# Performance work log

Hardware: AMD Instinct MI355X
Metric: run time of the kernel (lower is better)

## Reference

```python
import jax, jax.numpy as jnp
import numpy as np

D_MODEL = 1024
N_HEADS = 16
HEAD_SIZE = D_MODEL // N_HEADS
D_FF = 4096
EPS = 1e-6


def _layernorm(x, g, b):
    # Faithful to source: (x + mean) / (std + eps), unbiased std (torch default)
    mean = jnp.mean(x, axis=-1, keepdims=True)
    std = jnp.std(x, axis=-1, keepdims=True, ddof=1)
    return g * ((x + mean) / (std + EPS)) + b


def setup_inputs() -> dict:
    key = jax.random.key(0)
    ks = jax.random.split(key, 12)
    s = lambda fan_in: 1.0 / np.sqrt(fan_in)
    x = jax.random.normal(ks[0], (4, 2048, D_MODEL), dtype=jnp.float32)
    Wq = jax.random.uniform(ks[1], (N_HEADS, D_MODEL, HEAD_SIZE), jnp.float32, -s(D_MODEL), s(D_MODEL))
    Wk = jax.random.uniform(ks[2], (N_HEADS, D_MODEL, HEAD_SIZE), jnp.float32, -s(D_MODEL), s(D_MODEL))
    Wv = jax.random.uniform(ks[3], (N_HEADS, D_MODEL, HEAD_SIZE), jnp.float32, -s(D_MODEL), s(D_MODEL))
    Wo = jax.random.uniform(ks[4], (D_MODEL, D_MODEL), jnp.float32, -s(D_MODEL), s(D_MODEL))
    bo = jax.random.uniform(ks[5], (D_MODEL,), jnp.float32, -s(D_MODEL), s(D_MODEL))
    W1 = jax.random.uniform(ks[6], (D_MODEL, D_FF), jnp.float32, -s(D_MODEL), s(D_MODEL))
    b1 = jax.random.uniform(ks[7], (D_FF,), jnp.float32, -s(D_MODEL), s(D_MODEL))
    W2 = jax.random.uniform(ks[8], (D_FF, D_MODEL), jnp.float32, -s(D_FF), s(D_FF))
    b2 = jax.random.uniform(ks[9], (D_MODEL,), jnp.float32, -s(D_FF), s(D_FF))
    g1 = jnp.ones((D_MODEL,), jnp.float32)
    be1 = jnp.zeros((D_MODEL,), jnp.float32)
    g2 = jnp.ones((D_MODEL,), jnp.float32)
    be2 = jnp.zeros((D_MODEL,), jnp.float32)
    return {"x": x, "Wq": Wq, "Wk": Wk, "Wv": Wv, "Wo": Wo, "bo": bo,
            "W1": W1, "b1": b1, "W2": W2, "b2": b2,
            "g1": g1, "be1": be1, "g2": g2, "be2": be2}


def reference(x, Wq, Wk, Wv, Wo, bo, W1, b1, W2, b2, g1, be1, g2, be2):
    # Multi-head attention; note: source scales by sqrt(d_model), not sqrt(head_size)
    scale = 1.0 / np.sqrt(D_MODEL)
    q = jnp.einsum('bsd,hde->bhse', x, Wq)
    k = jnp.einsum('bsd,hde->bhse', x, Wk)
    v = jnp.einsum('bsd,hde->bhse', x, Wv)
    scores = jnp.einsum('bhse,bhte->bhst', q, k) * scale
    attn = jax.nn.softmax(scores, axis=-1)
    o = jnp.einsum('bhst,bhte->bhse', attn, v)
    B, H, S, E = o.shape
    o = o.transpose(0, 2, 1, 3).reshape(B, S, H * E)  # concat heads
    mha_out = o @ Wo + bo

    h1 = _layernorm(x + mha_out, g1, be1)

    ff = jax.nn.relu(h1 @ W1 + b1) @ W2 + b2
    out = _layernorm(h1 + ff, g2, be2)
    return out
```

## Files before the change

### kernel.cpp

```cpp
#include <hip/hip_runtime.h>

typedef short short8 __attribute__((ext_vector_type(8)));
typedef short short4v __attribute__((ext_vector_type(4)));
typedef float floatx4 __attribute__((ext_vector_type(4)));

#define D_MODEL 1024
#define N_HEADS 16
#define HEAD    64
#define D_FF    4096
#define SEQ     2048
#define BATCH   4
#define TOKENS  (BATCH*SEQ)

__device__ __forceinline__ float b2f(unsigned short u) {
  return __uint_as_float(((unsigned)u) << 16);
}
__device__ __forceinline__ unsigned short f2b(float f) {
  unsigned u = __float_as_uint(f);
  unsigned r = 0x7fffu + ((u >> 16) & 1u);
  return (unsigned short)((u + r) >> 16);
}
__device__ __forceinline__ floatx4 mfma16(short8 a, short8 b, floatx4 c) {
  return __builtin_amdgcn_mfma_f32_16x16x32_bf16(a, b, c, 0, 0, 0);
}
__device__ __forceinline__ void load16_lds(const unsigned short* g, unsigned short* l) {
  __builtin_amdgcn_global_load_lds((const __attribute__((address_space(1))) void*)g,
                                   (__attribute__((address_space(3))) void*)l, 16, 0, 0);
}

__device__ __forceinline__ void transp_body(
    const float* __restrict__ src, unsigned short* __restrict__ dst,
    int R, int C, int bx, int by, float (*t)[65])
{
  int cb = bx * 64, rb = by * 64;
#pragma unroll
  for (int i = 0; i < 16; i++) {
    int idx = i * 256 + threadIdx.x;
    int lr = idx >> 6, lc = idx & 63;
    t[lr][lc] = src[(size_t)(rb + lr) * C + cb + lc];
  }
  __syncthreads();
#pragma unroll
  for (int i = 0; i < 16; i++) {
    int idx = i * 256 + threadIdx.x;
    int lc = idx >> 6, lr = idx & 63;
    dst[(size_t)(cb + lc) * R + rb + lr] = f2b(t[lr][lc]);
  }
}

__global__ __launch_bounds__(256) void prep_kernel(
    const float* __restrict__ x, unsigned short* __restrict__ x_bf,
    const float* __restrict__ Wq, const float* __restrict__ Wk,
    const float* __restrict__ Wv, unsigned short* __restrict__ qkv_bt,
    const float* __restrict__ Wo, unsigned short* __restrict__ wo_bt,
    const float* __restrict__ W1, unsigned short* __restrict__ w1_bt,
    const float* __restrict__ W2, unsigned short* __restrict__ w2_bt)
{
  __shared__ float t[64][65];
  int bid = blockIdx.x;
  if (bid < 8192) {
    int idx = bid * 1024 + threadIdx.x * 4;
    float4 v = *(const float4*)(x + idx);
    short4v o;
    o[0] = (short)f2b(v.x); o[1] = (short)f2b(v.y);
    o[2] = (short)f2b(v.z); o[3] = (short)f2b(v.w);
    *(short4v*)(x_bf + idx) = o;
  } else if (bid < 8960) {
    int by = bid - 8192;
    int xt = by & 15, z = by >> 4;
    int sel = z >> 4, h = z & 15;
    const float* W = (sel == 0) ? Wq : ((sel == 1) ? Wk : Wv);
    const float* src = W + (size_t)h * D_MODEL * HEAD;
    int rb = xt * 64;
#pragma unroll
    for (int i = 0; i < 16; i++) {
      int idx = i * 256 + threadIdx.x;
      int lr = idx >> 6, lc = idx & 63;
      t[lr][lc] = src[(size_t)(rb + lr) * HEAD + lc];
    }
    __syncthreads();
    unsigned short* d0 = qkv_bt + (size_t)(sel * 1024 + h * 64) * D_MODEL;
#pragma unroll
    for (int i = 0; i < 16; i++) {
      int idx = i * 256 + threadIdx.x;
      int lc = idx >> 6, lr = idx & 63;
      d0[(size_t)lc * D_MODEL + rb + lr] = f2b(t[lr][lc]);
    }
  } else if (bid < 9216) {
    int i = bid - 8960;
    transp_body(Wo, wo_bt, 1024, 1024, i & 15, i >> 4, t);
  } else if (bid < 10240) {
    int i = bid - 9216;
    transp_body(W1, w1_bt, 1024, 4096, i & 63, i >> 6, t);
  } else {
    int i = bid - 10240;
    transp_body(W2, w2_bt, 4096, 1024, i & 15, i >> 4, t);
  }
}

__global__ __launch_bounds__(256, 2) void gemm128(
    const unsigned short* __restrict__ A, const unsigned short* __restrict__ BT,
    const float* __restrict__ biasf, const float* __restrict__ residf,
    const unsigned short* __restrict__ residb, void* __restrict__ outp,
    int M, int N, int K, int epi)
{
  __shared__ unsigned short a_sh[2 * 128 * 32];
  __shared__ unsigned short b_sh[2 * 128 * 32];

  const int tid  = threadIdx.x;
  const int lane = tid & 63;
  const int wave = tid >> 6;
  const int quad = lane >> 4;
  const int l15  = lane & 15;
  const int wm   = wave & 1;
  const int wn   = wave >> 1;

  const int lin = blockIdx.y * gridDim.x + blockIdx.x;
  const int xcd = lin & 7, j = lin >> 3;
  const int m0 = (xcd * 8 + (j & 7)) * 128;
  const int n0 = (j >> 3) * 128;

  const int rA = tid >> 2;
  const int kc = (tid & 3) * 8;
  const unsigned short* ag0 = A  + (size_t)(m0 + rA) * K + kc;
  const unsigned short* ag1 = A  + (size_t)(m0 + rA + 64) * K + kc;
  const unsigned short* bg0 = BT + (size_t)(n0 + rA) * K + kc;
  const unsigned short* bg1 = BT + (size_t)(n0 + rA + 64) * K + kc;
  unsigned short* la0 = a_sh + wave * 512;
  unsigned short* la1 = a_sh + 2048 + wave * 512;
  unsigned short* lb0 = b_sh + wave * 512;
  unsigned short* lb1 = b_sh + 2048 + wave * 512;

  floatx4 acc[4][4] = {};

  for (int k0 = 0; k0 < K; k0 += 64) {
    __syncthreads();
    load16_lds(ag0 + k0, la0);
    load16_lds(ag1 + k0, la1);
    load16_lds(bg0 + k0, lb0);
    load16_lds(bg1 + k0, lb1);
    load16_lds(ag0 + k0 + 32, la0 + 4096);
    load16_lds(ag1 + k0 + 32, la1 + 4096);
    load16_lds(bg0 + k0 + 32, lb0 + 4096);
    load16_lds(bg1 + k0 + 32, lb1 + 4096);
    __syncthreads();
#pragma unroll
    for (int h = 0; h < 2; h++) {
      short8 aF[4], bF[4];
#pragma unroll
      for (int i = 0; i < 4; i++)
        aF[i] = *(const short8*)(a_sh + h * 4096 + (wm * 64 + i * 16 + l15) * 32 + quad * 8);
#pragma unroll
      for (int i = 0; i < 4; i++)
        bF[i] = *(const short8*)(b_sh + h * 4096 + (wn * 64 + i * 16 + l15) * 32 + quad * 8);
#pragma unroll
      for (int mi = 0; mi < 4; mi++)
#pragma unroll
        for (int ni = 0; ni < 4; ni++)
          acc[mi][ni] = mfma16(aF[mi], bF[ni], acc[mi][ni]);
    }
  }

#pragma unroll
  for (int mi = 0; mi < 4; mi++) {
#pragma unroll
    for (int ni = 0; ni < 4; ni++) {
      const int col = n0 + wn * 64 + ni * 16 + l15;
      const int row0 = m0 + wm * 64 + mi * 16 + quad * 4;
      if (epi == 0) {
        int sel = col >> 10;
        int cc = col & 1023;
        int h = cc >> 6, e = cc & 63;
        int b = row0 >> 11, s0 = row0 & 2047;
        if (sel < 2) {
          unsigned short* base = (unsigned short*)outp + (size_t)sel * 8388608;
#pragma unroll
          for (int r = 0; r < 4; r++) {
            float v2 = (sel == 0) ? acc[mi][ni][r] * 0.04508422f : acc[mi][ni][r];
            base[((size_t)((b * N_HEADS + h) * SEQ + (s0 + r))) * HEAD + e] = f2b(v2);
          }
        } else {
          unsigned short* base = (unsigned short*)outp + (size_t)2 * 8388608;
          short4v pk;
#pragma unroll
          for (int r = 0; r < 4; r++) pk[r] = (short)f2b(acc[mi][ni][r]);
          *(short4v*)(base + ((size_t)((b * N_HEADS + h) * HEAD + e)) * SEQ + s0) = pk;
        }
      } else if (epi == 1) {
#pragma unroll
        for (int r = 0; r < 4; r++)
          ((float*)outp)[(size_t)(row0 + r) * N + col] =
              acc[mi][ni][r] + biasf[col] + residf[(size_t)(row0 + r) * N + col];
      } else if (epi == 2) {
#pragma unroll
        for (int r = 0; r < 4; r++)
          ((unsigned short*)outp)[(size_t)(row0 + r) * N + col] =
              f2b(fmaxf(acc[mi][ni][r] + biasf[col], 0.0f));
      } else {
#pragma unroll
        for (int r = 0; r < 4; r++)
          ((float*)outp)[(size_t)(row0 + r) * N + col] =
              acc[mi][ni][r] + biasf[col] + b2f(residb[(size_t)(row0 + r) * N + col]);
      }
    }
  }
}

__global__ __launch_bounds__(512, 2) void gemm256(
    const unsigned short* __restrict__ A, const unsigned short* __restrict__ BT,
    const float* __restrict__ biasf, void* __restrict__ outp,
    int M, int N, int K, int epi)
{
  __shared__ unsigned short a_sh[2 * 256 * 64];
  __shared__ unsigned short b_sh[2 * 256 * 64];

  const int tid  = threadIdx.x;
  const int lane = tid & 63;
  const int wave = tid >> 6;
  const int quad = lane >> 4;
  const int l15  = lane & 15;
  const int wm   = wave >> 2;
  const int wn   = wave & 3;

  const int lin = blockIdx.y * gridDim.x + blockIdx.x;
  const int xcd = lin & 7, j = lin >> 3;
  const int m0 = (xcd * 4 + (j & 3)) * 256;
  const int n0 = (j >> 2) * 256;

  const int u  = tid >> 3;
  const int sc = (tid & 7) ^ (u & 7);
  const unsigned short* a_src = A  + (size_t)(m0 + u) * K + sc * 8;
  const int borig = ((u >> 5) * 64) + (u & 31);
  const unsigned short* b_src = BT + (size_t)(n0 + borig) * K + sc * 8;
  unsigned short* a_dst = a_sh + wave * 512;
  unsigned short* b_dst = b_sh + wave * 512;

#define SA(T, Rc)  load16_lds(a_src + (size_t)(Rc) * K + (T) * 64, \
                              a_dst + ((T) & 1) * 16384 + (Rc) * 64)
#define SB(T, Rb, Radd) load16_lds(b_src + (size_t)(Radd) * K + (T) * 64, \
                              b_dst + ((T) & 1) * 16384 + (Rb) * 64)
#define STG_A0(T) do { SA(T, 0);   SA(T, 128); } while (0)
#define STG_A1(T) do { SA(T, 64);  SA(T, 192); } while (0)
#define STG_B0(T) do { SB(T, 0, 0);    SB(T, 64, 128); } while (0)
#define STG_B1(T) do { SB(T, 128, 32); SB(T, 192, 160); } while (0)

  floatx4 acc[8][4] = {};
  short8 aF[4][2];
  short8 bF[2][2][2];
  const unsigned short* ash = a_sh;
  const unsigned short* bsh = b_sh;

#define LDA(QM) \
  _Pragma("unroll") for (int mi = 0; mi < 4; mi++) \
  _Pragma("unroll") for (int kh = 0; kh < 2; kh++) \
    aF[mi][kh] = *(const short8*)(ash + (wm * 128 + (QM) * 64 + mi * 16 + l15) * 64 \
                                  + (((kh * 4 + quad) ^ (l15 & 7)) * 8));
#define LDB(QN) \
  _Pragma("unroll") for (int ni = 0; ni < 2; ni++) \
  _Pragma("unroll") for (int kh = 0; kh < 2; kh++) \
    bF[QN][ni][kh] = *(const short8*)(bsh + ((QN) * 128 + wn * 32 + ni * 16 + l15) * 64 \
                                      + (((kh * 4 + quad) ^ (l15 & 7)) * 8));
#define MM(QM, QN) \
  _Pragma("unroll") for (int mi = 0; mi < 4; mi++) \
  _Pragma("unroll") for (int ni = 0; ni < 2; ni++) { \
    acc[(QM) * 4 + mi][(QN) * 2 + ni] = \
        mfma16(aF[mi][0], bF[QN][ni][0], acc[(QM) * 4 + mi][(QN) * 2 + ni]); \
    acc[(QM) * 4 + mi][(QN) * 2 + ni] = \
        mfma16(aF[mi][1], bF[QN][ni][1], acc[(QM) * 4 + mi][(QN) * 2 + ni]); \
  }
#define PH_VM(N) asm volatile("s_waitcnt vmcnt(" #N ")" ::: "memory");
#define PH_MID() \
  __builtin_amdgcn_s_barrier(); \
  asm volatile("s_waitcnt lgkmcnt(0)" ::: "memory"); \
  __builtin_amdgcn_sched_barrier(0); \
  __builtin_amdgcn_s_setprio(1);
#define PH_END() \
  __builtin_amdgcn_s_setprio(0); \
  __builtin_amdgcn_s_barrier();

  const int NT = K >> 6;

  STG_A0(0); STG_B0(0); STG_A1(0); STG_B1(0); STG_A0(1); STG_B0(1);
  PH_VM(4)
  __builtin_amdgcn_s_barrier();

  for (int t = 0; t < NT - 2; ++t) {
    ash = a_sh + (t & 1) * 16384;
    bsh = b_sh + (t & 1) * 16384;

    LDA(0) LDB(0)
    STG_A1(t + 1);
    PH_MID() MM(0, 0) PH_END();

    LDB(1)
    STG_B1(t + 1);
    PH_MID() MM(0, 1) PH_END();

    LDA(1)
    STG_A0(t + 2);
    PH_MID() MM(1, 0) PH_END();

    STG_B0(t + 2);
    PH_VM(4)
    PH_MID() MM(1, 1) PH_END();
  }
  {
    const int t = NT - 2;
    ash = a_sh + (t & 1) * 16384;
    bsh = b_sh + (t & 1) * 16384;

    LDA(0) LDB(0)
    STG_A1(t + 1);
    PH_MID() MM(0, 0) PH_END();

    LDB(1)
    STG_B1(t + 1);
    PH_MID() MM(0, 1) PH_END();

    LDA(1)
    PH_MID() MM(1, 0) PH_END();

    PH_VM(0)
    PH_MID() MM(1, 1) PH_END();
  }
  {
    const int t = NT - 1;
    ash = a_sh + (t & 1) * 16384;
    bsh = b_sh + (t & 1) * 16384;

    LDA(0) LDB(0)
    PH_MID() MM(0, 0) PH_END();

    LDB(1)
    PH_MID() MM(0, 1) PH_END();

    LDA(1)
    PH_MID() MM(1, 0) PH_END();

    PH_MID() MM(1, 1) PH_END();
  }

#undef SA
#undef SB
#undef STG_A0
#undef STG_A1
#undef STG_B0
#undef STG_B1
#undef LDA
#undef LDB
#undef MM
#undef PH_VM
#undef PH_MID
#undef PH_END

#pragma unroll
  for (int mi = 0; mi < 8; mi++) {
#pragma unroll
    for (int ni = 0; ni < 4; ni++) {
      const int col = n0 + wn * 64 + ni * 16 + l15;
      const int row0 = m0 + wm * 128 + mi * 16 + quad * 4;
      if (epi == 0) {
        int sel = col >> 10;
        int cc = col & 1023;
        int h = cc >> 6, e = cc & 63;
        int b = row0 >> 11, s0 = row0 & 2047;
        if (sel < 2) {
          unsigned short* base = (unsigned short*)outp + (size_t)sel * 8388608;
#pragma unroll
          for (int r = 0; r < 4; r++) {
            float v2 = (sel == 0) ? acc[mi][ni][r] * 0.04508422f : acc[mi][ni][r];
            base[((size_t)((b * N_HEADS + h) * SEQ + (s0 + r))) * HEAD + e] = f2b(v2);
          }
        } else {
          unsigned short* base = (unsigned short*)outp + (size_t)2 * 8388608;
          short4v pk;
#pragma unroll
          for (int r = 0; r < 4; r++) pk[r] = (short)f2b(acc[mi][ni][r]);
          *(short4v*)(base + ((size_t)((b * N_HEADS + h) * HEAD + e)) * SEQ + s0) = pk;
        }
      } else {
#pragma unroll
        for (int r = 0; r < 4; r++)
          ((unsigned short*)outp)[(size_t)(row0 + r) * N + col] =
              f2b(fmaxf(acc[mi][ni][r] + biasf[col], 0.0f));
      }
    }
  }
}

__global__ __launch_bounds__(256, 4) void attn_kernel(
    const unsigned short* __restrict__ q, const unsigned short* __restrict__ k,
    const unsigned short* __restrict__ vt, unsigned short* __restrict__ o)
{
  const int bh = blockIdx.y;
  const int qt = blockIdx.x;
  const int tid = threadIdx.x, lane = tid & 63, wave = tid >> 6;
  const int quad = lane >> 4, l15 = lane & 15;
  const size_t base = (size_t)bh * SEQ * HEAD;

  __shared__ unsigned short k_sh[64 * 64];
  __shared__ unsigned short vT_sh[64 * 64];
  __shared__ unsigned short p_sh[4 * 32 * 72];
  unsigned short* pw = p_sh + wave * 32 * 72;

  short8 qf[2][2];
#pragma unroll
  for (int mj = 0; mj < 2; mj++) {
    const unsigned short* qp =
        q + base + (size_t)(qt * 128 + wave * 32 + mj * 16 + l15) * HEAD;
    qf[mj][0] = *(const short8*)(qp + quad * 8);
    qf[mj][1] = *(const short8*)(qp + 32 + quad * 8);
  }

  floatx4 oacc[2][4] = {};
  floatx4 rsacc[2] = {};

  short8 onesf;
  {
    short ov = (l15 == 0) ? (short)0x3F80 : (short)0;
#pragma unroll
    for (int jj = 0; jj < 8; jj++) onesf[jj] = ov;
  }

  const int r8 = lane >> 3, slot = lane & 7;

  for (int kt = 0; kt < SEQ / 64; kt++) {
    __syncthreads();
#pragma unroll
    for (int i = 0; i < 2; i++) {
      int t = wave * 16 + i * 8 + r8;
      int cg = slot ^ (t & 7);
      load16_lds(k + base + (size_t)(kt * 64 + t) * HEAD + cg * 8,
                 k_sh + (wave * 16 + i * 8) * 64);
      load16_lds(vt + base + (size_t)t * SEQ + kt * 64 + cg * 8,
                 vT_sh + (wave * 16 + i * 8) * 64);
    }
    __syncthreads();

#pragma unroll
    for (int ti = 0; ti < 4; ti++) {
      int t = ti * 16 + l15;
      short8 kf0 = *(const short8*)(k_sh + t * 64 + ((quad ^ (t & 7)) * 8));
      short8 kf1 = *(const short8*)(k_sh + t * 64 + (((4 + quad) ^ (t & 7)) * 8));
      floatx4 s0 = {0.f, 0.f, 0.f, 0.f}, s1 = {0.f, 0.f, 0.f, 0.f};
      __builtin_amdgcn_s_setprio(1);
      s0 = mfma16(kf0, qf[0][0], s0);
      s0 = mfma16(kf1, qf[0][1], s0);
      s1 = mfma16(kf0, qf[1][0], s1);
      s1 = mfma16(kf1, qf[1][1], s1);
      __builtin_amdgcn_s_setprio(0);
#pragma unroll
      for (int mj = 0; mj < 2; mj++) {
        floatx4 s = mj ? s1 : s0;
        float p0 = __builtin_amdgcn_exp2f(s[0]);
        float p1 = __builtin_amdgcn_exp2f(s[1]);
        float p2 = __builtin_amdgcn_exp2f(s[2]);
        float p3 = __builtin_amdgcn_exp2f(s[3]);
        uint2 u;
        u.x = __builtin_amdgcn_perm(__float_as_uint(p1), __float_as_uint(p0), 0x07060302u);
        u.y = __builtin_amdgcn_perm(__float_as_uint(p3), __float_as_uint(p2), 0x07060302u);
        *(uint2*)(pw + (mj * 16 + l15) * 72 + ti * 16 + quad * 4) = u;
      }
    }

    {
      short8 pf[2][2];
#pragma unroll
      for (int mj = 0; mj < 2; mj++) {
        pf[mj][0] = *(const short8*)(pw + (mj * 16 + l15) * 72 + quad * 8);
        pf[mj][1] = *(const short8*)(pw + (mj * 16 + l15) * 72 + 32 + quad * 8);
      }
      __builtin_amdgcn_s_setprio(1);
#pragma unroll
      for (int ni = 0; ni < 4; ni++) {
        int e = ni * 16 + l15;
        short8 bv0 = *(const short8*)(vT_sh + e * 64 + ((quad ^ (e & 7)) * 8));
        short8 bv1 = *(const short8*)(vT_sh + e * 64 + (((4 + quad) ^ (e & 7)) * 8));
#pragma unroll
        for (int mj = 0; mj < 2; mj++) {
          oacc[mj][ni] = mfma16(pf[mj][0], bv0, oacc[mj][ni]);
          oacc[mj][ni] = mfma16(pf[mj][1], bv1, oacc[mj][ni]);
        }
      }
#pragma unroll
      for (int mj = 0; mj < 2; mj++) {
        rsacc[mj] = mfma16(pf[mj][0], onesf, rsacc[mj]);
        rsacc[mj] = mfma16(pf[mj][1], onesf, rsacc[mj]);
      }
      __builtin_amdgcn_s_setprio(0);
    }
  }

  const int b = bh >> 4, h = bh & 15;
#pragma unroll
  for (int mj = 0; mj < 2; mj++)
#pragma unroll
    for (int r = 0; r < 4; r++) {
      int s = qt * 128 + wave * 32 + mj * 16 + quad * 4 + r;
      float rsv = __shfl(rsacc[mj][r], quad * 16, 64);
      float inv = 1.0f / rsv;
#pragma unroll
      for (int ni = 0; ni < 4; ni++)
        o[((size_t)(b * SEQ + s)) * D_MODEL + h * HEAD + ni * 16 + l15] =
            f2b(oacc[mj][ni][r] * inv);
    }
}

__global__ __launch_bounds__(256) void ln_kernel(
    const float* __restrict__ in, const float* __restrict__ g,
    const float* __restrict__ be, void* __restrict__ outp, int write_bf16)
{
  const int row = blockIdx.x * 4 + (threadIdx.x >> 6);
  const int lane = threadIdx.x & 63;
  const float* xp = in + (size_t)row * D_MODEL;
  float4 xv[4];
  float s = 0.0f, ss = 0.0f;
#pragma unroll
  for (int j = 0; j < 4; j++) {
    xv[j] = *(const float4*)(xp + j * 256 + lane * 4);
    s += (xv[j].x + xv[j].y) + (xv[j].z + xv[j].w);
    ss += (xv[j].x * xv[j].x + xv[j].y * xv[j].y) +
          (xv[j].z * xv[j].z + xv[j].w * xv[j].w);
  }
#pragma unroll
  for (int m = 1; m < 64; m <<= 1) {
    s += __shfl_xor(s, m, 64);
    ss += __shfl_xor(ss, m, 64);
  }
  float mean = s * (1.0f / 1024.0f);
  float var = fmaxf((ss - 1024.0f * mean * mean) * (1.0f / 1023.0f), 0.0f);
  float inv = 1.0f / (sqrtf(var) + 1e-6f);
#pragma unroll
  for (int j = 0; j < 4; j++) {
    int c = j * 256 + lane * 4;
    float4 g4 = *(const float4*)(g + c);
    float4 b4 = *(const float4*)(be + c);
    float y0 = g4.x * ((xv[j].x + mean) * inv) + b4.x;
    float y1 = g4.y * ((xv[j].y + mean) * inv) + b4.y;
    float y2 = g4.z * ((xv[j].z + mean) * inv) + b4.z;
    float y3 = g4.w * ((xv[j].w + mean) * inv) + b4.w;
    if (write_bf16) {
      short4v o4;
      o4[0] = (short)f2b(y0); o4[1] = (short)f2b(y1);
      o4[2] = (short)f2b(y2); o4[3] = (short)f2b(y3);
      *(short4v*)((unsigned short*)outp + (size_t)row * D_MODEL + c) = o4;
    } else {
      float4 o4 = {y0, y1, y2, y3};
      *(float4*)((float*)outp + (size_t)row * D_MODEL + c) = o4;
    }
  }
}

extern "C" void kernel_launch(void* const* d_in, const int* in_sizes, int n_in,
                              void* d_out, int out_size, void* d_ws, size_t ws_size,
                              hipStream_t stream)
{
  const float* x   = (const float*)d_in[0];
  const float* Wq  = (const float*)d_in[1];
  const float* Wk  = (const float*)d_in[2];
  const float* Wv  = (const float*)d_in[3];
  const float* Wo  = (const float*)d_in[4];
  const float* bo  = (const float*)d_in[5];
  const float* W1  = (const float*)d_in[6];
  const float* b1  = (const float*)d_in[7];
  const float* W2  = (const float*)d_in[8];
  const float* b2  = (const float*)d_in[9];
  const float* g1  = (const float*)d_in[10];
  const float* be1 = (const float*)d_in[11];
  const float* g2  = (const float*)d_in[12];
  const float* be2 = (const float*)d_in[13];
  float* out = (float*)d_out;

  unsigned short* ws     = (unsigned short*)d_ws;
  unsigned short* w1_bt  = ws;
  unsigned short* w2_bt  = ws + 4194304;
  unsigned short* qkv_bt = ws + 8388608;
  unsigned short* wo_bt  = ws + 11534336;
  unsigned short* x_bf   = ws + 12582912;
  unsigned short* qws    = ws + 20971520;
  unsigned short* kws    = ws + 29360128;
  unsigned short* vws    = ws + 37748736;
  unsigned short* ows    = x_bf;
  float*          r1     = (float*)(ws + 20971520);
  unsigned short* h1_bf  = x_bf;
  unsigned short* ff1    = ws + 20971520;

  dim3 blk(256);

  prep_kernel<<<11264, blk, 0, stream>>>(x, x_bf, Wq, Wk, Wv, qkv_bt,
                                         Wo, wo_bt, W1, w1_bt, W2, w2_bt);

  gemm256<<<dim3(3072 / 256, TOKENS / 256), dim3(512), 0, stream>>>(
      x_bf, qkv_bt, nullptr, qws, TOKENS, 3072, 1024, 0);
  attn_kernel<<<dim3(SEQ / 128, BATCH * N_HEADS), blk, 0, stream>>>(qws, kws, vws, ows);
  gemm128<<<dim3(1024 / 128, TOKENS / 128), blk, 0, stream>>>(
      ows, wo_bt, bo, x, nullptr, r1, TOKENS, 1024, 1024, 1);
  ln_kernel<<<TOKENS / 4, blk, 0, stream>>>(r1, g1, be1, h1_bf, 1);
  gemm256<<<dim3(4096 / 256, TOKENS / 256), dim3(512), 0, stream>>>(
      h1_bf, w1_bt, b1, ff1, TOKENS, 4096, 1024, 2);
  gemm128<<<dim3(1024 / 128, TOKENS / 128), blk, 0, stream>>>(
      ff1, w2_bt, b2, nullptr, h1_bf, out, TOKENS, 1024, 4096, 3);
  ln_kernel<<<TOKENS / 4, blk, 0, stream>>>(out, g2, be2, out, 0);
}
```

Measured before the change: 491.9 us.

## Replace gemm128 with pipelined 256x128 GEMM for output projection and FFN2

Replaces the simple 128x128 GEMM, which loads and then syncs each K-step, with a 256x128-tile, 512-thread kernel for the Wo and W2 projections (N=1024). The new kernel double-buffers LDS with XOR-swizzled layout to avoid bank conflicts, and splits each K-step into two phases. Each phase overlaps global-to-LDS prefetch of later tiles with MFMA work, using explicit vmcnt waits, barriers and setprio. This aims to hide memory latency and raise MFMA utilisation, at the cost of fewer blocks (256) on 256 CUs and more LDS per block.

New measurement: 470.8 us (median of 2 runs). 4.3% less time.

```diff
diff --git a/kernel.cpp b/kernel.cpp
--- a/kernel.cpp
+++ b/kernel.cpp
@@ -98,114 +98,6 @@
   }
 }
 
-__global__ __launch_bounds__(256, 2) void gemm128(
-    const unsigned short* __restrict__ A, const unsigned short* __restrict__ BT,
-    const float* __restrict__ biasf, const float* __restrict__ residf,
-    const unsigned short* __restrict__ residb, void* __restrict__ outp,
-    int M, int N, int K, int epi)
-{
-  __shared__ unsigned short a_sh[2 * 128 * 32];
-  __shared__ unsigned short b_sh[2 * 128 * 32];
-
-  const int tid  = threadIdx.x;
-  const int lane = tid & 63;
-  const int wave = tid >> 6;
-  const int quad = lane >> 4;
-  const int l15  = lane & 15;
-  const int wm   = wave & 1;
-  const int wn   = wave >> 1;
-
-  const int lin = blockIdx.y * gridDim.x + blockIdx.x;
-  const int xcd = lin & 7, j = lin >> 3;
-  const int m0 = (xcd * 8 + (j & 7)) * 128;
-  const int n0 = (j >> 3) * 128;
-
-  const int rA = tid >> 2;
-  const int kc = (tid & 3) * 8;
-  const unsigned short* ag0 = A  + (size_t)(m0 + rA) * K + kc;
-  const unsigned short* ag1 = A  + (size_t)(m0 + rA + 64) * K + kc;
-  const unsigned short* bg0 = BT + (size_t)(n0 + rA) * K + kc;
-  const unsigned short* bg1 = BT + (size_t)(n0 + rA + 64) * K + kc;
-  unsigned short* la0 = a_sh + wave * 512;
-  unsigned short* la1 = a_sh + 2048 + wave * 512;
-  unsigned short* lb0 = b_sh + wave * 512;
-  unsigned short* lb1 = b_sh + 2048 + wave * 512;
-
-  floatx4 acc[4][4] = {};
-
-  for (int k0 = 0; k0 < K; k0 += 64) {
-    __syncthreads();
-    load16_lds(ag0 + k0, la0);
-    load16_lds(ag1 + k0, la1);
-    load16_lds(bg0 + k0, lb0);
-    load16_lds(bg1 + k0, lb1);
-    load16_lds(ag0 + k0 + 32, la0 + 4096);
-    load16_lds(ag1 + k0 + 32, la1 + 4096);
-    load16_lds(bg0 + k0 + 32, lb0 + 4096);
-    load16_lds(bg1 + k0 + 32, lb1 + 4096);
-    __syncthreads();
-#pragma unroll
-    for (int h = 0; h < 2; h++) {
-      short8 aF[4], bF[4];
-#pragma unroll
-      for (int i = 0; i < 4; i++)
-        aF[i] = *(const short8*)(a_sh + h * 4096 + (wm * 64 + i * 16 + l15) * 32 + quad * 8);
-#pragma unroll
-      for (int i = 0; i < 4; i++)
-        bF[i] = *(const short8*)(b_sh + h * 4096 + (wn * 64 + i * 16 + l15) * 32 + quad * 8);
-#pragma unroll
-      for (int mi = 0; mi < 4; mi++)
-#pragma unroll
-        for (int ni = 0; ni < 4; ni++)
-          acc[mi][ni] = mfma16(aF[mi], bF[ni], acc[mi][ni]);
-    }
-  }
-
-#pragma unroll
-  for (int mi = 0; mi < 4; mi++) {
-#pragma unroll
-    for (int ni = 0; ni < 4; ni++) {
-      const int col = n0 + wn * 64 + ni * 16 + l15;
-      const int row0 = m0 + wm * 64 + mi * 16 + quad * 4;
-      if (epi == 0) {
-        int sel = col >> 10;
-        int cc = col & 1023;
-        int h = cc >> 6, e = cc & 63;
-        int b = row0 >> 11, s0 = row0 & 2047;
-        if (sel < 2) {
-          unsigned short* base = (unsigned short*)outp + (size_t)sel * 8388608;
-#pragma unroll
-          for (int r = 0; r < 4; r++) {
-            float v2 = (sel == 0) ? acc[mi][ni][r] * 0.04508422f : acc[mi][ni][r];
-            base[((size_t)((b * N_HEADS + h) * SEQ + (s0 + r))) * HEAD + e] = f2b(v2);
-          }
-        } else {
-          unsigned short* base = (unsigned short*)outp + (size_t)2 * 8388608;
-          short4v pk;
-#pragma unroll
-          for (int r = 0; r < 4; r++) pk[r] = (short)f2b(acc[mi][ni][r]);
-          *(short4v*)(base + ((size_t)((b * N_HEADS + h) * HEAD + e)) * SEQ + s0) = pk;
-        }
-      } else if (epi == 1) {
-#pragma unroll
-        for (int r = 0; r < 4; r++)
-          ((float*)outp)[(size_t)(row0 + r) * N + col] =
-              acc[mi][ni][r] + biasf[col] + residf[(size_t)(row0 + r) * N + col];
-      } else if (epi == 2) {
-#pragma unroll
-        for (int r = 0; r < 4; r++)
-          ((unsigned short*)outp)[(size_t)(row0 + r) * N + col] =
-              f2b(fmaxf(acc[mi][ni][r] + biasf[col], 0.0f));
-      } else {
-#pragma unroll
-        for (int r = 0; r < 4; r++)
-          ((float*)outp)[(size_t)(row0 + r) * N + col] =
-              acc[mi][ni][r] + biasf[col] + b2f(residb[(size_t)(row0 + r) * N + col]);
-      }
-    }
-  }
-}
-
 __global__ __launch_bounds__(512, 2) void gemm256(
     const unsigned short* __restrict__ A, const unsigned short* __restrict__ BT,
     const float* __restrict__ biasf, void* __restrict__ outp,
@@ -383,6 +275,155 @@
         for (int r = 0; r < 4; r++)
           ((unsigned short*)outp)[(size_t)(row0 + r) * N + col] =
               f2b(fmaxf(acc[mi][ni][r] + biasf[col], 0.0f));
+      }
+    }
+  }
+}
+
+__global__ __launch_bounds__(512, 2) void gemm256n(
+    const unsigned short* __restrict__ A, const unsigned short* __restrict__ BT,
+    const float* __restrict__ biasf, const float* __restrict__ residf,
+    const unsigned short* __restrict__ residb, void* __restrict__ outp,
+    int M, int N, int K, int epi)
+{
+  __shared__ unsigned short a_sh[2 * 256 * 64];
+  __shared__ unsigned short b_sh[2 * 128 * 64];
+
+  const int tid  = threadIdx.x;
+  const int lane = tid & 63;
+  const int wave = tid >> 6;
+  const int quad = lane >> 4;
+  const int l15  = lane & 15;
+  const int wm   = wave >> 1;
+  const int wn   = wave & 1;
+
+  const int lin = blockIdx.y * gridDim.x + blockIdx.x;
+  const int xcd = lin & 7, j = lin >> 3;
+  const int m0 = (xcd * 4 + (j & 3)) * 256;
+  const int n0 = (j >> 2) * 128;
+
+  const int u  = tid >> 3;
+  const int sc = (tid & 7) ^ (u & 7);
+  const unsigned short* a_src = A  + (size_t)(m0 + u) * K + sc * 8;
+  const unsigned short* b_src = BT + (size_t)(n0 + u) * K + sc * 8;
+  unsigned short* a_dst = a_sh + wave * 512;
+  unsigned short* b_dst = b_sh + wave * 512;
+
+#define SA(T, Rc) load16_lds(a_src + (size_t)(Rc) * K + (T) * 64, \
+                             a_dst + ((T) & 1) * 16384 + (Rc) * 64)
+#define SB(T, Rb) load16_lds(b_src + (size_t)(Rb) * K + (T) * 64, \
+                             b_dst + ((T) & 1) * 8192 + (Rb) * 64)
+#define STG_A0(T) do { SA(T, 0);   SA(T, 64);  } while (0)
+#define STG_A1(T) do { SA(T, 128); SA(T, 192); } while (0)
+#define STG_B(T)  do { SB(T, 0);   SB(T, 64);  } while (0)
+
+  floatx4 acc[4][4] = {};
+  short8 aF[2][2];
+  short8 bF[2][2][2];
+  const unsigned short* ash = a_sh;
+  const unsigned short* bsh = b_sh;
+
+#define LDA(QM) \
+  _Pragma("unroll") for (int mi = 0; mi < 2; mi++) \
+  _Pragma("unroll") for (int kh = 0; kh < 2; kh++) \
+    aF[mi][kh] = *(const short8*)(ash + ((QM) * 128 + wm * 32 + mi * 16 + l15) * 64 \
+                                  + (((kh * 4 + quad) ^ (l15 & 7)) * 8));
+#define LDB(QN) \
+  _Pragma("unroll") for (int ni = 0; ni < 2; ni++) \
+  _Pragma("unroll") for (int kh = 0; kh < 2; kh++) \
+    bF[QN][ni][kh] = *(const short8*)(bsh + ((QN) * 64 + wn * 32 + ni * 16 + l15) * 64 \
+                                      + (((kh * 4 + quad) ^ (l15 & 7)) * 8));
+#define MM2(QM) \
+  _Pragma("unroll") for (int qn = 0; qn < 2; qn++) \
+  _Pragma("unroll") for (int mi = 0; mi < 2; mi++) \
+  _Pragma("unroll") for (int ni = 0; ni < 2; ni++) { \
+    acc[(QM) * 2 + mi][qn * 2 + ni] = \
+        mfma16(aF[mi][0], bF[qn][ni][0], acc[(QM) * 2 + mi][qn * 2 + ni]); \
+    acc[(QM) * 2 + mi][qn * 2 + ni] = \
+        mfma16(aF[mi][1], bF[qn][ni][1], acc[(QM) * 2 + mi][qn * 2 + ni]); \
+  }
+#define PH_VM(N) asm volatile("s_waitcnt vmcnt(" #N ")" ::: "memory");
+#define PH_MID() \
+  __builtin_amdgcn_s_barrier(); \
+  asm volatile("s_waitcnt lgkmcnt(0)" ::: "memory"); \
+  __builtin_amdgcn_sched_barrier(0); \
+  __builtin_amdgcn_s_setprio(1);
+#define PH_END() \
+  __builtin_amdgcn_s_setprio(0); \
+  __builtin_amdgcn_s_barrier();
+
+  const int NT = K >> 6;
+
+  STG_A0(0); STG_B(0); STG_A1(0); STG_A0(1); STG_B(1);
+  PH_VM(4)
+  __builtin_amdgcn_s_barrier();
+
+  for (int t = 0; t < NT - 2; ++t) {
+    ash = a_sh + (t & 1) * 16384;
+    bsh = b_sh + (t & 1) * 8192;
+
+    LDA(0) LDB(0) LDB(1)
+    STG_A1(t + 1);
+    PH_MID() MM2(0) PH_END();
+
+    LDA(1)
+    STG_A0(t + 2); STG_B(t + 2);
+    PH_VM(4)
+    PH_MID() MM2(1) PH_END();
+  }
+  {
+    const int t = NT - 2;
+    ash = a_sh + (t & 1) * 16384;
+    bsh = b_sh + (t & 1) * 8192;
+
+    LDA(0) LDB(0) LDB(1)
+    STG_A1(t + 1);
+    PH_MID() MM2(0) PH_END();
+
+    LDA(1)
+    PH_VM(0)
+    PH_MID() MM2(1) PH_END();
+  }
+  {
+    const int t = NT - 1;
+    ash = a_sh + (t & 1) * 16384;
+    bsh = b_sh + (t & 1) * 8192;
+
+    LDA(0) LDB(0) LDB(1)
+    PH_MID() MM2(0) PH_END();
+
+    LDA(1)
+    PH_MID() MM2(1) PH_END();
+  }
+
+#undef SA
+#undef SB
+#undef STG_A0
+#undef STG_A1
+#undef STG_B
+#undef LDA
+#undef LDB
+#undef MM2
+#undef PH_VM
+#undef PH_MID
+#undef PH_END
+
+#pragma unroll
+  for (int am = 0; am < 4; am++) {
+    const int row0 = m0 + (am >> 1) * 128 + wm * 32 + (am & 1) * 16 + quad * 4;
+#pragma unroll
+    for (int bn = 0; bn < 4; bn++) {
+      const int col = n0 + (bn >> 1) * 64 + wn * 32 + (bn & 1) * 16 + l15;
+      if (epi == 1) {
+#pragma unroll
+        for (int r = 0; r < 4; r++)
+          ((float*)outp)[(size_t)(row0 + r) * N + col] =
+              acc[am][bn][r] + biasf[col] + residf[(size_t)(row0 + r) * N + col];
+      } else {
+#pragma unroll
+        for (int r = 0; r < 4; r++)
+          ((float*)outp)[(size_t)(row0 + r) * N + col] =
+              acc[am][bn][r] + biasf[col] + b2f(residb[(size_t)(row0 + r) * N + col]);
       }
     }
   }
@@ -593,12 +634,12 @@
   gemm256<<<dim3(3072 / 256, TOKENS / 256), dim3(512), 0, stream>>>(
       x_bf, qkv_bt, nullptr, qws, TOKENS, 3072, 1024, 0);
   attn_kernel<<<dim3(SEQ / 128, BATCH * N_HEADS), blk, 0, stream>>>(qws, kws, vws, ows);
-  gemm128<<<dim3(1024 / 128, TOKENS / 128), blk, 0, stream>>>(
+  gemm256n<<<dim3(1024 / 128, TOKENS / 256), dim3(512), 0, stream>>>(
       ows, wo_bt, bo, x, nullptr, r1, TOKENS, 1024, 1024, 1);
   ln_kernel<<<TOKENS / 4, blk, 0, stream>>>(r1, g1, be1, h1_bf, 1);
   gemm256<<<dim3(4096 / 256, TOKENS / 256), dim3(512), 0, stream>>>(
       h1_bf, w1_bt, b1, ff1, TOKENS, 4096, 1024, 2);
-  gemm128<<<dim3(1024 / 128, TOKENS / 128), blk, 0, stream>>>(
+  gemm256n<<<dim3(1024 / 128, TOKENS / 256), dim3(512), 0, stream>>>(
       ff1, w2_bt, b2, nullptr, h1_bf, out, TOKENS, 1024, 4096, 3);
   ln_kernel<<<TOKENS / 4, blk, 0, stream>>>(out, g2, be2, out, 0);
 }
```
